# Performance work log

Measured on AMD Instinct MI355X. Metric: run time of the kernel, lower is better.

## Reference

```python
import jax, jax.numpy as jnp
import numpy as np

HID = 512

def setup_inputs() -> dict:
    key = jax.random.key(0)
    k1, k2, k3, k4, k5, k6 = jax.random.split(key, 6)
    B, T, H = 32, 4096, HID
    enc_seq = jax.random.normal(k1, (B, T, H), dtype=jnp.float32)
    enc_mask = jax.random.randint(k2, (B, T), 0, 2, dtype=jnp.int32)
    dec_state = jax.random.normal(k3, (B, H), dtype=jnp.float32)
    # Linear weights, torch layout: y = x @ W.T
    scale = 1.0 / np.sqrt(H)
    W_h = jax.random.uniform(k4, (H, H), jnp.float32, -scale, scale)
    W_s = jax.random.uniform(k5, (H, H), jnp.float32, -scale, scale)
    v = jax.random.uniform(k6, (H,), jnp.float32, -scale, scale)
    return {"enc_seq": enc_seq, "enc_mask": enc_mask, "dec_state": dec_state,
            "W_h": W_h, "W_s": W_s, "v": v}

def reference(enc_seq, enc_mask, dec_state, W_h, W_s, v):
    # s: [B,H] -> [B,1,H] broadcast over T; h: [B,T,H]
    s = jnp.einsum('bh,kh->bk', dec_state, W_s)[:, None, :]
    h = jnp.einsum('bth,kh->btk', enc_seq, W_h)
    e = jnp.einsum('bth,h->bt', jnp.tanh(h + s), v)  # [B,T]
    e = jnp.where(enc_mask == 0, jnp.float32(-1e9), e)
    a = jax.nn.softmax(e, axis=1)  # [B,T]
    ctx = jnp.einsum('bt,bth->bh', a, enc_seq)  # [B,H]
    return (ctx, a)
```

## Files before the change

### kernel.cpp

```cpp
#include <hip/hip_runtime.h>
#include <hip/hip_bf16.h>
#include <cstdint>
#include <cstddef>

#define HID 512
#define T_SZ 4096

typedef __bf16 bf16x8 __attribute__((ext_vector_type(8)));
typedef float f32x4 __attribute__((ext_vector_type(4)));

__device__ __forceinline__ unsigned short f2bf_rne(float f) {
    unsigned int u = __float_as_uint(f);
    unsigned int r = (u + 0x7FFFu + ((u >> 16) & 1u)) >> 16;
    return (unsigned short)r;
}

__device__ __forceinline__ float fast_tanh(float x) {
    float e = __expf(2.0f * x);
    return 1.0f - 2.0f / (e + 1.0f);
}

__device__ __forceinline__ void gload_lds16(const void* g, void* l) {
    __builtin_amdgcn_global_load_lds(
        (const __attribute__((address_space(1))) unsigned int*)g,
        (__attribute__((address_space(3))) unsigned int*)l, 16, 0, 0);
}

__global__ void k_s(const float* __restrict__ dec, const float* __restrict__ Ws,
                    float* __restrict__ s) {
    int idx = blockIdx.x * 256 + threadIdx.x;
    int b = idx >> 9, n = idx & 511;
    const float4* dp = reinterpret_cast<const float4*>(dec + (size_t)b * HID);
    const float4* wp = reinterpret_cast<const float4*>(Ws + (size_t)n * HID);
    float acc = 0.f;
#pragma unroll 8
    for (int i = 0; i < HID / 4; ++i) {
        float4 d = dp[i], w = wp[i];
        acc += d.x * w.x + d.y * w.y + d.z * w.z + d.w * w.w;
    }
    s[idx] = acc;
}

__global__ void k_pack(const float* __restrict__ Wh, uint4* __restrict__ Wb) {
    int idx = blockIdx.x * 256 + threadIdx.x;
    int n = idx >> 6;
    int k0 = (idx & 63) * 8;
    const float4* p = reinterpret_cast<const float4*>(Wh + (size_t)n * HID + k0);
    float4 x0 = p[0], x1 = p[1];
    uint4 w;
    w.x = f2bf_rne(x0.x) | ((unsigned)f2bf_rne(x0.y) << 16);
    w.y = f2bf_rne(x0.z) | ((unsigned)f2bf_rne(x0.w) << 16);
    w.z = f2bf_rne(x1.x) | ((unsigned)f2bf_rne(x1.y) << 16);
    w.w = f2bf_rne(x1.z) | ((unsigned)f2bf_rne(x1.w) << 16);
    int n4 = n >> 4, c = n & 15, kk = k0 >> 5, g = (k0 >> 3) & 3;
    Wb[(size_t)kk * 2048 + n4 * 64 + g * 16 + c] = w;
}

__global__ void __launch_bounds__(512, 2) k_gemm_e(
    const float* __restrict__ enc, const uint4* __restrict__ Wb,
    const float* __restrict__ s, const float* __restrict__ v,
    float* __restrict__ e_out) {
    __shared__ __align__(16) unsigned char Abuf[2][4096];
    __shared__ __align__(16) unsigned char Bbuf[2][32768];

    const int tid = threadIdx.x;
    const int lane = tid & 63, wid = tid >> 6;
    const int c16 = lane & 15, g4 = lane >> 4;
    const size_t row0 = (size_t)blockIdx.x * 64;
    const int b = (int)(row0 >> 12);

    float sv_s[4], sv_v[4];
#pragma unroll
    for (int ni = 0; ni < 4; ++ni) {
        int n = (wid * 4 + ni) * 16 + c16;
        sv_s[ni] = s[b * HID + n];
        sv_v[ni] = v[n];
    }

    const int ac = tid >> 1, hh = tid & 1;
    const int amrow = ((ac >> 6) << 4) + (ac & 15);
    const int ak = ((ac >> 4) & 3) * 8 + hh * 4;
    const float* Ag = enc + (row0 + amrow) * HID + ak;
    const int abyte = ac * 16 + hh * 8;

    const uint4* Bsrc = Wb + wid * 64 + lane;

#pragma unroll
    for (int q = 0; q < 4; ++q)
        gload_lds16(Bsrc + q * 512, &Bbuf[0][(q * 512 + wid * 64) * 16]);
    float4 a0 = *reinterpret_cast<const float4*>(Ag);
    float4 aR[2];
    aR[1] = *reinterpret_cast<const float4*>(Ag + 32);
    {
        uint2 w;
        w.x = f2bf_rne(a0.x) | ((unsigned)f2bf_rne(a0.y) << 16);
        w.y = f2bf_rne(a0.z) | ((unsigned)f2bf_rne(a0.w) << 16);
        *reinterpret_cast<uint2*>(&Abuf[0][abyte]) = w;
    }
    asm volatile("s_waitcnt vmcnt(1) lgkmcnt(0)\n\ts_barrier" ::: "memory");

    f32x4 acc[4][4] = {};

#pragma unroll
    for (int kk = 0; kk < 16; ++kk) {
        if (kk < 15) {
            float4 x = aR[(kk + 1) & 1];
            uint2 w;
            w.x = f2bf_rne(x.x) | ((unsigned)f2bf_rne(x.y) << 16);
            w.y = f2bf_rne(x.z) | ((unsigned)f2bf_rne(x.w) << 16);
            *reinterpret_cast<uint2*>(&Abuf[(kk + 1) & 1][abyte]) = w;
#pragma unroll
            for (int q = 0; q < 4; ++q)
                gload_lds16(Bsrc + (size_t)(kk + 1) * 2048 + q * 512,
                            &Bbuf[(kk + 1) & 1][(q * 512 + wid * 64) * 16]);
        }
        if (kk < 14)
            aR[kk & 1] = *reinterpret_cast<const float4*>(Ag + (kk + 2) * 32);

        bf16x8 af[4], bf[4];
#pragma unroll
        for (int mi = 0; mi < 4; ++mi)
            af[mi] = *reinterpret_cast<const bf16x8*>(
                &Abuf[kk & 1][(mi * 64 + lane) * 16]);
#pragma unroll
        for (int ni = 0; ni < 4; ++ni)
            bf[ni] = *reinterpret_cast<const bf16x8*>(
                &Bbuf[kk & 1][((wid * 4 + ni) * 64 + lane) * 16]);
#pragma unroll
        for (int mi = 0; mi < 4; ++mi)
#pragma unroll
            for (int ni = 0; ni < 4; ++ni)
                acc[mi][ni] = __builtin_amdgcn_mfma_f32_16x16x32_bf16(
                    af[mi], bf[ni], acc[mi][ni], 0, 0, 0);

        if (kk < 14)
            asm volatile("s_waitcnt vmcnt(1) lgkmcnt(0)\n\ts_barrier" ::: "memory");
        else if (kk == 14)
            asm volatile("s_waitcnt vmcnt(0) lgkmcnt(0)\n\ts_barrier" ::: "memory");
    }

    float e_part[4][4] = {};
#pragma unroll
    for (int ni = 0; ni < 4; ++ni) {
        float sn = sv_s[ni], vn = sv_v[ni];
#pragma unroll
        for (int mi = 0; mi < 4; ++mi)
#pragma unroll
            for (int r = 0; r < 4; ++r)
                e_part[mi][r] += fast_tanh(acc[mi][ni][r] + sn) * vn;
    }
#pragma unroll
    for (int mm = 1; mm <= 8; mm <<= 1)
#pragma unroll
        for (int mi = 0; mi < 4; ++mi)
#pragma unroll
            for (int r = 0; r < 4; ++r)
                e_part[mi][r] += __shfl_xor(e_part[mi][r], mm);

    __syncthreads();
    float* red = reinterpret_cast<float*>(&Abuf[0][0]);
    if (c16 == 0) {
#pragma unroll
        for (int mi = 0; mi < 4; ++mi)
#pragma unroll
            for (int r = 0; r < 4; ++r)
                red[wid * 64 + mi * 16 + g4 * 4 + r] = e_part[mi][r];
    }
    __syncthreads();
    if (tid < 64) {
        float sum = 0.f;
#pragma unroll
        for (int w = 0; w < 8; ++w) sum += red[w * 64 + tid];
        e_out[row0 + tid] = sum;
    }
}

__global__ void k_softmax(float* __restrict__ ea, const int* __restrict__ mask) {
    int b = blockIdx.x, tid = threadIdx.x;
    int lane = tid & 63, wid = tid >> 6;
    __shared__ float red[16];
    float vals[4]; int ms[4];
    float mx = -1e30f;
#pragma unroll
    for (int j = 0; j < 4; ++j) {
        size_t t = (size_t)b * T_SZ + tid + j * 1024;
        vals[j] = ea[t];
        ms[j] = mask[t];
        if (ms[j]) mx = fmaxf(mx, vals[j]);
    }
#pragma unroll
    for (int m = 32; m >= 1; m >>= 1) mx = fmaxf(mx, __shfl_xor(mx, m));
    if (lane == 0) red[wid] = mx;
    __syncthreads();
    if (tid == 0) {
        float m2 = red[0];
        for (int i = 1; i < 16; ++i) m2 = fmaxf(m2, red[i]);
        red[0] = m2;
    }
    __syncthreads();
    mx = red[0];
    __syncthreads();
    float pv[4]; float sum = 0.f;
#pragma unroll
    for (int j = 0; j < 4; ++j) { pv[j] = ms[j] ? __expf(vals[j] - mx) : 0.f; sum += pv[j]; }
#pragma unroll
    for (int m = 32; m >= 1; m >>= 1) sum += __shfl_xor(sum, m);
    if (lane == 0) red[wid] = sum;
    __syncthreads();
    if (tid == 0) {
        float s2 = 0.f;
        for (int i = 0; i < 16; ++i) s2 += red[i];
        red[0] = s2;
    }
    __syncthreads();
    float inv = 1.f / red[0];
#pragma unroll
    for (int j = 0; j < 4; ++j) {
        size_t t = (size_t)b * T_SZ + tid + j * 1024;
        ea[t] = pv[j] * inv;
    }
}

__global__ void k_ctx(const float* __restrict__ enc, const float* __restrict__ a,
                      float2* __restrict__ part) {
    int ts = blockIdx.x, b = blockIdx.y, tid = threadIdx.x;
    size_t rbase = (size_t)b * T_SZ + (size_t)ts * 128;
    const float2* ep = reinterpret_cast<const float2*>(enc + rbase * HID) + tid;
    const float* ap = a + rbase;
    float ax = 0.f, ay = 0.f, bx = 0.f, by = 0.f;
#pragma unroll 2
    for (int t = 0; t < 128; t += 2) {
        float a0 = ap[t], a1 = ap[t + 1];
        float2 e0 = ep[(size_t)t * 256], e1 = ep[(size_t)(t + 1) * 256];
        ax += a0 * e0.x; ay += a0 * e0.y;
        bx += a1 * e1.x; by += a1 * e1.y;
    }
    float2 r; r.x = ax + bx; r.y = ay + by;
    part[(size_t)(b * 32 + ts) * 256 + tid] = r;
}

__global__ void k_ctxred(const float* __restrict__ part, float* __restrict__ ctx) {
    int idx = blockIdx.x * 256 + threadIdx.x;
    int b = idx >> 9, h = idx & 511;
    float sum = 0.f;
#pragma unroll
    for (int ts = 0; ts < 32; ++ts) sum += part[(size_t)(b * 32 + ts) * 512 + h];
    ctx[idx] = sum;
}

extern "C" void kernel_launch(void* const* d_in, const int* in_sizes, int n_in,
                              void* d_out, int out_size, void* d_ws, size_t ws_size,
                              hipStream_t stream) {
    const float* enc  = (const float*)d_in[0];
    const int*   mask = (const int*)d_in[1];
    const float* dec  = (const float*)d_in[2];
    const float* Wh   = (const float*)d_in[3];
    const float* Ws   = (const float*)d_in[4];
    const float* v    = (const float*)d_in[5];

    float* out = (float*)d_out;
    float* ctx = out;
    float* a   = out + 16384;

    float* ws   = (float*)d_ws;
    float* s    = ws;
    uint4* Wb   = (uint4*)(ws + 16384);
    float* part = ws + 16384 + 131072;

    hipLaunchKernelGGL(k_s,      dim3(64),      dim3(256),  0, stream, dec, Ws, s);
    hipLaunchKernelGGL(k_pack,   dim3(128),     dim3(256),  0, stream, Wh, Wb);
    hipLaunchKernelGGL(k_gemm_e, dim3(2048),    dim3(512),  0, stream, enc, Wb, s, v, a);
    hipLaunchKernelGGL(k_softmax,dim3(32),      dim3(1024), 0, stream, a, mask);
    hipLaunchKernelGGL(k_ctx,    dim3(32, 32),  dim3(256),  0, stream, enc, a, (float2*)part);
    hipLaunchKernelGGL(k_ctxred, dim3(64),      dim3(256),  0, stream, part, ctx);
}
```

Before: 186.3 us.

## Double GEMM row tile to 128 with 2x4 warp layout and deeper A prefetch

```diff
diff --git a/kernel.cpp b/kernel.cpp
--- a/kernel.cpp
+++ b/kernel.cpp
@@ -13,6 +13,13 @@
     unsigned int u = __float_as_uint(f);
     unsigned int r = (u + 0x7FFFu + ((u >> 16) & 1u)) >> 16;
     return (unsigned short)r;
+}
+
+__device__ __forceinline__ bf16x8 pack8(float4 x0, float4 x1) {
+    bf16x8 r;
+    r[0] = (__bf16)x0.x; r[1] = (__bf16)x0.y; r[2] = (__bf16)x0.z; r[3] = (__bf16)x0.w;
+    r[4] = (__bf16)x1.x; r[5] = (__bf16)x1.y; r[6] = (__bf16)x1.z; r[7] = (__bf16)x1.w;
+    return r;
 }
 
 __device__ __forceinline__ float fast_tanh(float x) {
@@ -60,88 +67,89 @@
     const float* __restrict__ enc, const uint4* __restrict__ Wb,
     const float* __restrict__ s, const float* __restrict__ v,
     float* __restrict__ e_out) {
-    __shared__ __align__(16) unsigned char Abuf[2][4096];
+    __shared__ __align__(16) unsigned char Abuf[2][8192];
     __shared__ __align__(16) unsigned char Bbuf[2][32768];
+    __shared__ float red[4][2][64];
 
     const int tid = threadIdx.x;
+    const int p = blockIdx.x;
+    const int logical = (p & 7) * 128 + (p >> 3);
+    const size_t row0 = (size_t)logical * 128;
+    const int b = (int)(row0 >> 12);
+
     const int lane = tid & 63, wid = tid >> 6;
     const int c16 = lane & 15, g4 = lane >> 4;
-    const size_t row0 = (size_t)blockIdx.x * 64;
-    const int b = (int)(row0 >> 12);
-
-    float sv_s[4], sv_v[4];
-#pragma unroll
-    for (int ni = 0; ni < 4; ++ni) {
-        int n = (wid * 4 + ni) * 16 + c16;
+    const int wm = wid >> 2, wn = wid & 3;
+
+    const int arow = ((tid >> 6) << 4) + (tid & 15);
+    const int ak = ((tid >> 4) & 3) * 8;
+    const float* Ag = enc + (row0 + arow) * HID + ak;
+    const int abyte = tid * 16;
+
+    const uint4* Bs = Wb + wid * 256 + lane;
+
+    float4 aR[3][2];
+
+#pragma unroll
+    for (int r = 0; r < 4; ++r)
+        gload_lds16(Bs + r * 64, &Bbuf[0][(wid * 256 + r * 64 + lane) * 16]);
+    float4 t0 = *reinterpret_cast<const float4*>(Ag);
+    float4 t1 = *reinterpret_cast<const float4*>(Ag + 4);
+    aR[1][0] = *reinterpret_cast<const float4*>(Ag + 32);
+    aR[1][1] = *reinterpret_cast<const float4*>(Ag + 36);
+    aR[2][0] = *reinterpret_cast<const float4*>(Ag + 64);
+    aR[2][1] = *reinterpret_cast<const float4*>(Ag + 68);
+    *reinterpret_cast<bf16x8*>(&Abuf[0][abyte]) = pack8(t0, t1);
+    asm volatile("s_waitcnt lgkmcnt(0)\n\ts_barrier" ::: "memory");
+
+    f32x4 acc[4][8] = {};
+
+#pragma unroll
+    for (int kk = 0; kk < 16; ++kk) {
+        if (kk + 1 <= 15) {
+#pragma unroll
+            for (int r = 0; r < 4; ++r)
+                gload_lds16(Bs + (size_t)(kk + 1) * 2048 + r * 64,
+                            &Bbuf[(kk + 1) & 1][(wid * 256 + r * 64 + lane) * 16]);
+        }
+        if (kk + 3 <= 15) {
+            aR[kk % 3][0] = *reinterpret_cast<const float4*>(Ag + (kk + 3) * 32);
+            aR[kk % 3][1] = *reinterpret_cast<const float4*>(Ag + (kk + 3) * 32 + 4);
+        }
+        if (kk + 1 <= 15)
+            *reinterpret_cast<bf16x8*>(&Abuf[(kk + 1) & 1][abyte]) =
+                pack8(aR[(kk + 1) % 3][0], aR[(kk + 1) % 3][1]);
+        bf16x8 af[4], bf[8];
+#pragma unroll
+        for (int mi = 0; mi < 4; ++mi)
+            af[mi] = *reinterpret_cast<const bf16x8*>(
+                &Abuf[kk & 1][((wm * 4 + mi) * 64 + lane) * 16]);
+#pragma unroll
+        for (int ni = 0; ni < 8; ++ni)
+            bf[ni] = *reinterpret_cast<const bf16x8*>(
+                &Bbuf[kk & 1][((wn * 8 + ni) * 64 + lane) * 16]);
+#pragma unroll
+        for (int mi = 0; mi < 4; ++mi)
+#pragma unroll
+            for (int ni = 0; ni < 8; ++ni)
+                acc[mi][ni] = __builtin_amdgcn_mfma_f32_16x16x32_bf16(
+                    af[mi], bf[ni], acc[mi][ni], 0, 0, 0);
+        if (kk <= 12)
+            asm volatile("s_waitcnt vmcnt(2) lgkmcnt(0)\n\ts_barrier" ::: "memory");
+        else if (kk <= 14)
+            asm volatile("s_waitcnt vmcnt(0) lgkmcnt(0)\n\ts_barrier" ::: "memory");
+    }
+
+    float sv_s[8], sv_v[8];
+#pragma unroll
+    for (int ni = 0; ni < 8; ++ni) {
+        int n = (wn * 8 + ni) * 16 + c16;
         sv_s[ni] = s[b * HID + n];
         sv_v[ni] = v[n];
     }
-
-    const int ac = tid >> 1, hh = tid & 1;
-    const int amrow = ((ac >> 6) << 4) + (ac & 15);
-    const int ak = ((ac >> 4) & 3) * 8 + hh * 4;
-    const float* Ag = enc + (row0 + amrow) * HID + ak;
-    const int abyte = ac * 16 + hh * 8;
-
-    const uint4* Bsrc = Wb + wid * 64 + lane;
-
-#pragma unroll
-    for (int q = 0; q < 4; ++q)
-        gload_lds16(Bsrc + q * 512, &Bbuf[0][(q * 512 + wid * 64) * 16]);
-    float4 a0 = *reinterpret_cast<const float4*>(Ag);
-    float4 aR[2];
-    aR[1] = *reinterpret_cast<const float4*>(Ag + 32);
-    {
-        uint2 w;
-        w.x = f2bf_rne(a0.x) | ((unsigned)f2bf_rne(a0.y) << 16);
-        w.y = f2bf_rne(a0.z) | ((unsigned)f2bf_rne(a0.w) << 16);
-        *reinterpret_cast<uint2*>(&Abuf[0][abyte]) = w;
-    }
-    asm volatile("s_waitcnt vmcnt(1) lgkmcnt(0)\n\ts_barrier" ::: "memory");
-
-    f32x4 acc[4][4] = {};
-
-#pragma unroll
-    for (int kk = 0; kk < 16; ++kk) {
-        if (kk < 15) {
-            float4 x = aR[(kk + 1) & 1];
-            uint2 w;
-            w.x = f2bf_rne(x.x) | ((unsigned)f2bf_rne(x.y) << 16);
-            w.y = f2bf_rne(x.z) | ((unsigned)f2bf_rne(x.w) << 16);
-            *reinterpret_cast<uint2*>(&Abuf[(kk + 1) & 1][abyte]) = w;
-#pragma unroll
-            for (int q = 0; q < 4; ++q)
-                gload_lds16(Bsrc + (size_t)(kk + 1) * 2048 + q * 512,
-                            &Bbuf[(kk + 1) & 1][(q * 512 + wid * 64) * 16]);
-        }
-        if (kk < 14)
-            aR[kk & 1] = *reinterpret_cast<const float4*>(Ag + (kk + 2) * 32);
-
-        bf16x8 af[4], bf[4];
-#pragma unroll
-        for (int mi = 0; mi < 4; ++mi)
-            af[mi] = *reinterpret_cast<const bf16x8*>(
-                &Abuf[kk & 1][(mi * 64 + lane) * 16]);
-#pragma unroll
-        for (int ni = 0; ni < 4; ++ni)
-            bf[ni] = *reinterpret_cast<const bf16x8*>(
-                &Bbuf[kk & 1][((wid * 4 + ni) * 64 + lane) * 16]);
-#pragma unroll
-        for (int mi = 0; mi < 4; ++mi)
-#pragma unroll
-            for (int ni = 0; ni < 4; ++ni)
-                acc[mi][ni] = __builtin_amdgcn_mfma_f32_16x16x32_bf16(
-                    af[mi], bf[ni], acc[mi][ni], 0, 0, 0);
-
-        if (kk < 14)
-            asm volatile("s_waitcnt vmcnt(1) lgkmcnt(0)\n\ts_barrier" ::: "memory");
-        else if (kk == 14)
-            asm volatile("s_waitcnt vmcnt(0) lgkmcnt(0)\n\ts_barrier" ::: "memory");
-    }
-
     float e_part[4][4] = {};
 #pragma unroll
-    for (int ni = 0; ni < 4; ++ni) {
+    for (int ni = 0; ni < 8; ++ni) {
         float sn = sv_s[ni], vn = sv_v[ni];
 #pragma unroll
         for (int mi = 0; mi < 4; ++mi)
@@ -158,20 +166,18 @@
                 e_part[mi][r] += __shfl_xor(e_part[mi][r], mm);
 
     __syncthreads();
-    float* red = reinterpret_cast<float*>(&Abuf[0][0]);
     if (c16 == 0) {
 #pragma unroll
         for (int mi = 0; mi < 4; ++mi)
 #pragma unroll
             for (int r = 0; r < 4; ++r)
-                red[wid * 64 + mi * 16 + g4 * 4 + r] = e_part[mi][r];
-    }
-    __syncthreads();
-    if (tid < 64) {
-        float sum = 0.f;
-#pragma unroll
-        for (int w = 0; w < 8; ++w) sum += red[w * 64 + tid];
-        e_out[row0 + tid] = sum;
+                red[wn][wm][mi * 16 + g4 * 4 + r] = e_part[mi][r];
+    }
+    __syncthreads();
+    if (tid < 128) {
+        int wm2 = tid >> 6, idx = tid & 63;
+        e_out[row0 + wm2 * 64 + idx] =
+            red[0][wm2][idx] + red[1][wm2][idx] + red[2][wm2][idx] + red[3][wm2][idx];
     }
 }
 
@@ -269,7 +275,7 @@
 
     hipLaunchKernelGGL(k_s,      dim3(64),      dim3(256),  0, stream, dec, Ws, s);
     hipLaunchKernelGGL(k_pack,   dim3(128),     dim3(256),  0, stream, Wh, Wb);
-    hipLaunchKernelGGL(k_gemm_e, dim3(2048),    dim3(512),  0, stream, enc, Wb, s, v, a);
+    hipLaunchKernelGGL(k_gemm_e, dim3(1024),    dim3(512),  0, stream, enc, Wb, s, v, a);
     hipLaunchKernelGGL(k_softmax,dim3(32),      dim3(1024), 0, stream, a, mask);
     hipLaunchKernelGGL(k_ctx,    dim3(32, 32),  dim3(256),  0, stream, enc, a, (float2*)part);
     hipLaunchKernelGGL(k_ctxred, dim3(64),      dim3(256),  0, stream, part, ctx);
```

Result: slower. 193.1 us (+3.6%).
